# Kernel optimization log

Measured on AMD Instinct MI355X. Metric: run time of the kernel, lower is better.

The kernel has to match this reference:

```python
import jax, jax.numpy as jnp
import numpy as np

TEMPERATURE = 0.5
EPSILON = 1e-9


def _l2_normalize(x, eps=1e-12):
    # matches torch F.normalize(p=2, dim=-1): x / max(||x||, eps)
    n = jnp.linalg.norm(x, axis=-1, keepdims=True)
    return x / jnp.maximum(n, eps)


def setup_inputs() -> dict:
    key = jax.random.key(0)
    k1, k2, k3 = jax.random.split(key, 3)
    N, D, V = 8192, 128, 3
    H_consensus = jax.random.normal(k1, (N, D), dtype=jnp.float32)
    S_similarity = jax.random.uniform(k2, (N, N), dtype=jnp.float32)
    H_views = jax.random.normal(k3, (V, N, D), dtype=jnp.float32)
    return {"H_consensus": H_consensus, "S_similarity": S_similarity, "H_views": H_views}


def reference(H_consensus, S_similarity, H_views):
    N = H_consensus.shape[0]
    V = H_views.shape[0]
    Hc = _l2_normalize(H_consensus)            # [N, D]
    Hv = _l2_normalize(H_views)                # [V, N, D]
    sim = jnp.einsum('nd,vmd->vnm', Hc, Hv)    # [V, N, N]
    positive = jnp.diagonal(sim, axis1=1, axis2=2) / TEMPERATURE  # [V, N]
    weights = 1.0 - S_similarity               # [N, N], broadcast over V
    denom = jnp.sum(weights * jnp.exp(sim / TEMPERATURE), axis=-1)  # [V, N]
    denom = jnp.maximum(denom, EPSILON)
    loss = -(positive - jnp.log(denom))        # [V, N]
    return jnp.sum(loss) / (N * V)
```

## Files before the change

kernel.cpp:

```cpp
#include <hip/hip_runtime.h>
#include <hip/hip_bf16.h>

constexpr int kN = 8192;
constexpr int kD = 128;
constexpr int kV = 3;
constexpr int kNV = kV * kN;
constexpr int kNChunk = 512;
constexpr int kNTile = 32;
constexpr int kIters = kNChunk / kNTile;
constexpr int kAccStride = 529;
constexpr float kLn2 = 0.6931471805599453f;
constexpr float kScaleHc = 2.885390081777927f;

typedef __attribute__((ext_vector_type(8))) short bf16x8;
typedef __attribute__((ext_vector_type(4))) float floatx4;

#if __has_builtin(__builtin_amdgcn_exp2f)
#define EXP2F(x) __builtin_amdgcn_exp2f(x)
#else
#define EXP2F(x) exp2f(x)
#endif

__device__ __forceinline__ unsigned pack_bf16(float a, float b) {
    unsigned ua = __float_as_uint(a);
    unsigned ub = __float_as_uint(b);
    ua = (ua + 0x7FFFu + ((ua >> 16) & 1u)) >> 16;
    ub = (ub + 0x7FFFu + ((ub >> 16) & 1u)) >> 16;
    return ua | (ub << 16);
}

__device__ __forceinline__ float quad_sum(float p) {
    float t = p;
    asm("v_permlane16_swap_b32 %0, %1" : "+v"(p), "+v"(t));
    p += t;
    t = p;
    asm("v_permlane32_swap_b32 %0, %1" : "+v"(p), "+v"(t));
    return p + t;
}

__global__ void k_normalize(const float* __restrict__ Hc, const float* __restrict__ Hv,
                            unsigned* __restrict__ HcB, unsigned* __restrict__ HvB) {
    int row  = (blockIdx.x * blockDim.x + threadIdx.x) >> 6;
    int lane = threadIdx.x & 63;
    const float* src;
    unsigned* dst;
    float extra;
    if (row < kN) { src = Hc + (size_t)row * kD; dst = HcB + (size_t)row * (kD / 2); extra = kScaleHc; }
    else {
        int r = row - kN;
        src = Hv + (size_t)r * kD; dst = HvB + (size_t)r * (kD / 2); extra = 1.0f;
    }
    float2 x = ((const float2*)src)[lane];
    float ss = x.x * x.x + x.y * x.y;
    ss += __shfl_xor(ss, 1);  ss += __shfl_xor(ss, 2);  ss += __shfl_xor(ss, 4);
    ss += __shfl_xor(ss, 8);  ss += __shfl_xor(ss, 16); ss += __shfl_xor(ss, 32);
    float inv = extra * rsqrtf(fmaxf(ss, 1e-24f));
    dst[lane] = pack_bf16(x.x * inv, x.y * inv);
}

__global__ void k_positive(const unsigned* __restrict__ HcB, const unsigned* __restrict__ HvB,
                           float* __restrict__ pos_partial) {
    int row  = (blockIdx.x * blockDim.x + threadIdx.x) >> 6;
    int lane = threadIdx.x & 63;
    int w    = threadIdx.x >> 6;
    int n    = row & (kN - 1);
    unsigned a = HcB[(size_t)n * (kD / 2) + lane];
    unsigned b = HvB[(size_t)row * (kD / 2) + lane];
    float dot = __uint_as_float(a << 16) * __uint_as_float(b << 16)
              + __uint_as_float(a & 0xFFFF0000u) * __uint_as_float(b & 0xFFFF0000u);
    dot += __shfl_xor(dot, 1);  dot += __shfl_xor(dot, 2);  dot += __shfl_xor(dot, 4);
    dot += __shfl_xor(dot, 8);  dot += __shfl_xor(dot, 16); dot += __shfl_xor(dot, 32);
    __shared__ float acc4[4];
    if (lane == 0) acc4[w] = dot;
    __syncthreads();
    if (threadIdx.x == 0)
        atomicAdd(&pos_partial[blockIdx.x & 255], acc4[0] + acc4[1] + acc4[2] + acc4[3]);
}

__launch_bounds__(256, 3)
__global__ void k_main(const unsigned* __restrict__ HcB, const unsigned* __restrict__ HvB,
                       const float* __restrict__ S, float* __restrict__ denom) {
    __shared__ short Htile[2][kNTile * 136];
    __shared__ float accum[4 * kV * kAccStride];

    const int tid  = threadIdx.x;
    const int w    = tid >> 6;
    const int lane = tid & 63;
    const int col  = lane & 15;
    const int quad = lane >> 4;
    const int m0b  = blockIdx.x * 64;
    const int m0w  = m0b + w * 16;
    const int nbase = blockIdx.y * kNChunk;
    const int sr = tid >> 4;
    const int sc = tid & 15;

    bf16x8 afrag[kV][4];
#pragma unroll
    for (int v = 0; v < kV; ++v) {
        const short* rowp = (const short*)HvB + ((size_t)(v * kN + m0w + col)) * kD;
#pragma unroll
        for (int kk = 0; kk < 4; ++kk)
            afrag[v][kk] = *(const bf16x8*)(rowp + kk * 32 + quad * 8);
    }

    const short* hc = (const short*)HcB;
    const float* Sp = S + (size_t)(nbase + col) * kN + m0b + (w << 4) + (quad << 2);

    {
        float4 ha = *(const float4*)(hc + (size_t)(nbase + sr) * kD + sc * 8);
        float4 hb = *(const float4*)(hc + (size_t)(nbase + sr + 16) * kD + sc * 8);
        *(float4*)&Htile[0][sr * 136 + sc * 8]        = ha;
        *(float4*)&Htile[0][(sr + 16) * 136 + sc * 8] = hb;
    }
    float4 s0 = *(const float4*)(Sp);
    float4 s1 = *(const float4*)(Sp + (size_t)16 * kN);
    __syncthreads();

    for (int it = 0; it < kIters; ++it) {
        int itn = (it + 1 < kIters) ? it + 1 : it;
        int n0n = nbase + itn * kNTile;
        float4 ha  = *(const float4*)(hc + (size_t)(n0n + sr) * kD + sc * 8);
        float4 hb  = *(const float4*)(hc + (size_t)(n0n + sr + 16) * kD + sc * 8);
        float4 s0n = *(const float4*)(Sp + (size_t)(itn * 32) * kN);
        float4 s1n = *(const float4*)(Sp + (size_t)(itn * 32 + 16) * kN);

        const int cur = it & 1;
#pragma unroll
        for (int sub = 0; sub < 2; ++sub) {
            const int nrow = sub * 16 + col;
            bf16x8 bfrag[4];
#pragma unroll
            for (int kk = 0; kk < 4; ++kk)
                bfrag[kk] = *(const bf16x8*)&Htile[cur][nrow * 136 + kk * 32 + quad * 8];
            float4 s4 = sub ? s1 : s0;

            floatx4 acc0 = {0.f,0.f,0.f,0.f}, acc1 = {0.f,0.f,0.f,0.f}, acc2 = {0.f,0.f,0.f,0.f};
#pragma unroll
            for (int kk = 0; kk < 4; ++kk) {
                acc0 = __builtin_amdgcn_mfma_f32_16x16x32_bf16(afrag[0][kk], bfrag[kk], acc0, 0, 0, 0);
                acc1 = __builtin_amdgcn_mfma_f32_16x16x32_bf16(afrag[1][kk], bfrag[kk], acc1, 0, 0, 0);
                acc2 = __builtin_amdgcn_mfma_f32_16x16x32_bf16(afrag[2][kk], bfrag[kk], acc2, 0, 0, 0);
            }
            float w0 = 1.f - s4.x, w1 = 1.f - s4.y, w2 = 1.f - s4.z, w3 = 1.f - s4.w;
            float p0 = w0 * EXP2F(acc0[0]) + w1 * EXP2F(acc0[1]) + w2 * EXP2F(acc0[2]) + w3 * EXP2F(acc0[3]);
            float p1 = w0 * EXP2F(acc1[0]) + w1 * EXP2F(acc1[1]) + w2 * EXP2F(acc1[2]) + w3 * EXP2F(acc1[3]);
            float p2 = w0 * EXP2F(acc2[0]) + w1 * EXP2F(acc2[1]) + w2 * EXP2F(acc2[2]) + w3 * EXP2F(acc2[3]);
            p0 = quad_sum(p0);
            p1 = quad_sum(p1);
            p2 = quad_sum(p2);
            float val = (quad == 0) ? p0 : ((quad == 1) ? p1 : p2);
            if (quad < 3)
                accum[(w * kV + quad) * kAccStride + it * kNTile + sub * 16 + col] = val;
        }

        s0 = s0n; s1 = s1n;
        const int nxt = cur ^ 1;
        *(float4*)&Htile[nxt][sr * 136 + sc * 8]        = ha;
        *(float4*)&Htile[nxt][(sr + 16) * 136 + sc * 8] = hb;
        __syncthreads();
    }

    for (int i = tid; i < kV * kNChunk; i += 256) {
        int v = i >> 9, c = i & (kNChunk - 1);
        float sum = accum[(0 * kV + v) * kAccStride + c]
                  + accum[(1 * kV + v) * kAccStride + c]
                  + accum[(2 * kV + v) * kAccStride + c]
                  + accum[(3 * kV + v) * kAccStride + c];
        atomicAdd(&denom[(size_t)v * kN + nbase + c], sum);
    }
}

__global__ void k_final(const float* __restrict__ denom, const float* __restrict__ pos_partial,
                        float* __restrict__ out) {
    int idx  = blockIdx.x * 256 + threadIdx.x;
    int lane = threadIdx.x & 63;
    int w    = threadIdx.x >> 6;
    float val = logf(fmaxf(denom[idx], 1e-9f));
    if (blockIdx.x == 0) val -= pos_partial[threadIdx.x] * kLn2;
    val += __shfl_xor(val, 1);  val += __shfl_xor(val, 2);  val += __shfl_xor(val, 4);
    val += __shfl_xor(val, 8);  val += __shfl_xor(val, 16); val += __shfl_xor(val, 32);
    __shared__ float acc4[4];
    if (lane == 0) acc4[w] = val;
    __syncthreads();
    if (threadIdx.x == 0)
        atomicAdd(out, (acc4[0] + acc4[1] + acc4[2] + acc4[3]) * (1.0f / kNV));
}

extern "C" void kernel_launch(void* const* d_in, const int* in_sizes, int n_in,
                              void* d_out, int out_size, void* d_ws, size_t ws_size,
                              hipStream_t stream) {
    const float* Hc = (const float*)d_in[0];
    const float* S  = (const float*)d_in[1];
    const float* Hv = (const float*)d_in[2];

    unsigned* HcB  = (unsigned*)d_ws;
    unsigned* HvB  = HcB + (size_t)kN * (kD / 2);
    float*    den  = (float*)(HvB + (size_t)kV * kN * (kD / 2));
    float*    posp = den + kNV;
    float*    outF = (float*)d_out;

    hipMemsetAsync(den, 0, ((size_t)kNV + 256) * sizeof(float), stream);
    hipMemsetAsync(outF, 0, sizeof(float), stream);

    k_normalize<<<dim3((kN + kV * kN) / 4), 256, 0, stream>>>(Hc, Hv, HcB, HvB);
    k_positive<<<dim3(kNV / 4), 256, 0, stream>>>(HcB, HvB, posp);
    k_main<<<dim3(kN / 64, kN / kNChunk), dim3(256), 0, stream>>>(HcB, HvB, S, den);
    k_final<<<dim3(kNV / 256), dim3(256), 0, stream>>>(den, posp, outF);
}
```

Baseline: 407.9 us.

## Switch main kernel to 32x32x16 MFMA with 128-wide M tiles per block

Moves the main similarity kernel from 16x16x32 to 32x32x16 bf16 MFMA tiles. Each wave now owns 32 columns of m, so a block covers 128 columns, and each loaded Hc tile is reused across twice as many columns. The cross-lane reduction shrinks to a single permlane32 swap, and each wave makes one LDS B-fragment read per k-step. In exchange, registers grow (24 A fragments plus 48 accumulators), so occupancy drops to 2 blocks per SIMD and the grid is halved, which may reduce latency hiding.

```diff
diff --git a/kernel.cpp b/kernel.cpp
--- a/kernel.cpp
+++ b/kernel.cpp
@@ -6,14 +6,15 @@
 constexpr int kV = 3;
 constexpr int kNV = kV * kN;
 constexpr int kNChunk = 512;
-constexpr int kNTile = 32;
-constexpr int kIters = kNChunk / kNTile;
-constexpr int kAccStride = 529;
+constexpr int kMTile = 128;
+constexpr int kRows = 32;
+constexpr int kIters = kNChunk / kRows;
+constexpr int kAccStride = 520;
 constexpr float kLn2 = 0.6931471805599453f;
 constexpr float kScaleHc = 2.885390081777927f;
 
 typedef __attribute__((ext_vector_type(8))) short bf16x8;
-typedef __attribute__((ext_vector_type(4))) float floatx4;
+typedef __attribute__((ext_vector_type(16))) float floatx16;
 
 #if __has_builtin(__builtin_amdgcn_exp2f)
 #define EXP2F(x) __builtin_amdgcn_exp2f(x)
@@ -29,11 +30,8 @@
     return ua | (ub << 16);
 }
 
-__device__ __forceinline__ float quad_sum(float p) {
+__device__ __forceinline__ float half_sum(float p) {
     float t = p;
-    asm("v_permlane16_swap_b32 %0, %1" : "+v"(p), "+v"(t));
-    p += t;
-    t = p;
     asm("v_permlane32_swap_b32 %0, %1" : "+v"(p), "+v"(t));
     return p + t;
 }
@@ -77,34 +75,34 @@
         atomicAdd(&pos_partial[blockIdx.x & 255], acc4[0] + acc4[1] + acc4[2] + acc4[3]);
 }
 
-__launch_bounds__(256, 3)
+__launch_bounds__(256, 2)
 __global__ void k_main(const unsigned* __restrict__ HcB, const unsigned* __restrict__ HvB,
                        const float* __restrict__ S, float* __restrict__ denom) {
-    __shared__ short Htile[2][kNTile * 136];
+    __shared__ short Htile[2][kRows * 136];
     __shared__ float accum[4 * kV * kAccStride];
 
     const int tid  = threadIdx.x;
     const int w    = tid >> 6;
     const int lane = tid & 63;
-    const int col  = lane & 15;
-    const int quad = lane >> 4;
-    const int m0b  = blockIdx.x * 64;
-    const int m0w  = m0b + w * 16;
+    const int l31  = lane & 31;
+    const int kh   = lane >> 5;
+    const int m0b  = blockIdx.x * kMTile;
+    const int m0w  = m0b + w * 32;
     const int nbase = blockIdx.y * kNChunk;
     const int sr = tid >> 4;
     const int sc = tid & 15;
 
-    bf16x8 afrag[kV][4];
+    bf16x8 afrag[kV][8];
 #pragma unroll
     for (int v = 0; v < kV; ++v) {
-        const short* rowp = (const short*)HvB + ((size_t)(v * kN + m0w + col)) * kD;
-#pragma unroll
-        for (int kk = 0; kk < 4; ++kk)
-            afrag[v][kk] = *(const bf16x8*)(rowp + kk * 32 + quad * 8);
+        const short* rowp = (const short*)HvB + ((size_t)(v * kN + m0w + l31)) * kD + kh * 8;
+#pragma unroll
+        for (int ks = 0; ks < 8; ++ks)
+            afrag[v][ks] = *(const bf16x8*)(rowp + ks * 16);
     }
 
     const short* hc = (const short*)HcB;
-    const float* Sp = S + (size_t)(nbase + col) * kN + m0b + (w << 4) + (quad << 2);
+    const float* Sp = S + (size_t)(nbase + l31) * kN + m0w + (kh << 2);
 
     {
         float4 ha = *(const float4*)(hc + (size_t)(nbase + sr) * kD + sc * 8);
@@ -112,48 +110,53 @@
         *(float4*)&Htile[0][sr * 136 + sc * 8]        = ha;
         *(float4*)&Htile[0][(sr + 16) * 136 + sc * 8] = hb;
     }
-    float4 s0 = *(const float4*)(Sp);
-    float4 s1 = *(const float4*)(Sp + (size_t)16 * kN);
+    float4 sg0 = *(const float4*)(Sp);
+    float4 sg1 = *(const float4*)(Sp + 8);
+    float4 sg2 = *(const float4*)(Sp + 16);
+    float4 sg3 = *(const float4*)(Sp + 24);
     __syncthreads();
 
     for (int it = 0; it < kIters; ++it) {
         int itn = (it + 1 < kIters) ? it + 1 : it;
-        int n0n = nbase + itn * kNTile;
+        int n0n = nbase + itn * kRows;
         float4 ha  = *(const float4*)(hc + (size_t)(n0n + sr) * kD + sc * 8);
         float4 hb  = *(const float4*)(hc + (size_t)(n0n + sr + 16) * kD + sc * 8);
-        float4 s0n = *(const float4*)(Sp + (size_t)(itn * 32) * kN);
-        float4 s1n = *(const float4*)(Sp + (size_t)(itn * 32 + 16) * kN);
+        const float* Spn = Sp + (size_t)(itn * kRows) * kN;
+        float4 sn0 = *(const float4*)(Spn);
+        float4 sn1 = *(const float4*)(Spn + 8);
+        float4 sn2 = *(const float4*)(Spn + 16);
+        float4 sn3 = *(const float4*)(Spn + 24);
 
         const int cur = it & 1;
-#pragma unroll
-        for (int sub = 0; sub < 2; ++sub) {
-            const int nrow = sub * 16 + col;
-            bf16x8 bfrag[4];
-#pragma unroll
-            for (int kk = 0; kk < 4; ++kk)
-                bfrag[kk] = *(const bf16x8*)&Htile[cur][nrow * 136 + kk * 32 + quad * 8];
-            float4 s4 = sub ? s1 : s0;
-
-            floatx4 acc0 = {0.f,0.f,0.f,0.f}, acc1 = {0.f,0.f,0.f,0.f}, acc2 = {0.f,0.f,0.f,0.f};
-#pragma unroll
-            for (int kk = 0; kk < 4; ++kk) {
-                acc0 = __builtin_amdgcn_mfma_f32_16x16x32_bf16(afrag[0][kk], bfrag[kk], acc0, 0, 0, 0);
-                acc1 = __builtin_amdgcn_mfma_f32_16x16x32_bf16(afrag[1][kk], bfrag[kk], acc1, 0, 0, 0);
-                acc2 = __builtin_amdgcn_mfma_f32_16x16x32_bf16(afrag[2][kk], bfrag[kk], acc2, 0, 0, 0);
-            }
+        floatx16 a0 = {0.f}, a1 = {0.f}, a2 = {0.f};
+#pragma unroll
+        for (int ks = 0; ks < 8; ++ks) {
+            bf16x8 bfrag = *(const bf16x8*)&Htile[cur][l31 * 136 + ks * 16 + kh * 8];
+            a0 = __builtin_amdgcn_mfma_f32_32x32x16_bf16(afrag[0][ks], bfrag, a0, 0, 0, 0);
+            a1 = __builtin_amdgcn_mfma_f32_32x32x16_bf16(afrag[1][ks], bfrag, a1, 0, 0, 0);
+            a2 = __builtin_amdgcn_mfma_f32_32x32x16_bf16(afrag[2][ks], bfrag, a2, 0, 0, 0);
+        }
+
+        float p0 = 0.f, p1 = 0.f, p2 = 0.f;
+#pragma unroll
+        for (int g = 0; g < 4; ++g) {
+            float4 s4 = (g == 0) ? sg0 : (g == 1) ? sg1 : (g == 2) ? sg2 : sg3;
             float w0 = 1.f - s4.x, w1 = 1.f - s4.y, w2 = 1.f - s4.z, w3 = 1.f - s4.w;
-            float p0 = w0 * EXP2F(acc0[0]) + w1 * EXP2F(acc0[1]) + w2 * EXP2F(acc0[2]) + w3 * EXP2F(acc0[3]);
-            float p1 = w0 * EXP2F(acc1[0]) + w1 * EXP2F(acc1[1]) + w2 * EXP2F(acc1[2]) + w3 * EXP2F(acc1[3]);
-            float p2 = w0 * EXP2F(acc2[0]) + w1 * EXP2F(acc2[1]) + w2 * EXP2F(acc2[2]) + w3 * EXP2F(acc2[3]);
-            p0 = quad_sum(p0);
-            p1 = quad_sum(p1);
-            p2 = quad_sum(p2);
-            float val = (quad == 0) ? p0 : ((quad == 1) ? p1 : p2);
-            if (quad < 3)
-                accum[(w * kV + quad) * kAccStride + it * kNTile + sub * 16 + col] = val;
+            p0 += w0 * EXP2F(a0[g*4+0]) + w1 * EXP2F(a0[g*4+1]) + w2 * EXP2F(a0[g*4+2]) + w3 * EXP2F(a0[g*4+3]);
+            p1 += w0 * EXP2F(a1[g*4+0]) + w1 * EXP2F(a1[g*4+1]) + w2 * EXP2F(a1[g*4+2]) + w3 * EXP2F(a1[g*4+3]);
+            p2 += w0 * EXP2F(a2[g*4+0]) + w1 * EXP2F(a2[g*4+1]) + w2 * EXP2F(a2[g*4+2]) + w3 * EXP2F(a2[g*4+3]);
         }
-
-        s0 = s0n; s1 = s1n;
+        p0 = half_sum(p0);
+        p1 = half_sum(p1);
+        p2 = half_sum(p2);
+        if (lane < 32) {
+            float* slot = &accum[(w * kV) * kAccStride + it * kRows + l31];
+            slot[0 * kAccStride] = p0;
+            slot[1 * kAccStride] = p1;
+            slot[2 * kAccStride] = p2;
+        }
+
+        sg0 = sn0; sg1 = sn1; sg2 = sn2; sg3 = sn3;
         const int nxt = cur ^ 1;
         *(float4*)&Htile[nxt][sr * 136 + sc * 8]        = ha;
         *(float4*)&Htile[nxt][(sr + 16) * 136 + sc * 8] = hb;
@@ -204,6 +207,6 @@
 
     k_normalize<<<dim3((kN + kV * kN) / 4), 256, 0, stream>>>(Hc, Hv, HcB, HvB);
     k_positive<<<dim3(kNV / 4), 256, 0, stream>>>(HcB, HvB, posp);
-    k_main<<<dim3(kN / 64, kN / kNChunk), dim3(256), 0, stream>>>(HcB, HvB, S, den);
+    k_main<<<dim3(kN / kMTile, kN / kNChunk), dim3(256), 0, stream>>>(HcB, HvB, S, den);
     k_final<<<dim3(kNV / 256), dim3(256), 0, stream>>>(den, posp, outF);
 }
```

After: 397.5 us. 2.5% less time.
